# Optimization experiments

Hardware: AMD Instinct MI355X
Metric: run time of the kernel (lower is better)

The kernel has to match this reference:

```python
import jax, jax.numpy as jnp
import numpy as np

B, S, D, H = 4, 2048, 2048, 16
HD = D // H  # 128
THETA = 10000.0


def setup_inputs() -> dict:
    key = jax.random.key(0)
    k1, k2, k3 = jax.random.split(key, 3)
    x = jax.random.normal(k1, (B, S, D), dtype=jnp.float32)
    wqkv = jax.random.normal(k2, (3 * D, D), dtype=jnp.float32) * (1.0 / np.sqrt(D))
    wo = jax.random.normal(k3, (D, D), dtype=jnp.float32) * (1.0 / np.sqrt(D))
    return {"x": x, "wqkv": wqkv, "wo": wo}


def _rotate_half(t):
    t1 = t[..., : t.shape[-1] // 2]
    t2 = t[..., t.shape[-1] // 2 :]
    return jnp.concatenate([-t2, t1], axis=-1)


def reference(x, wqkv, wo):
    b, s, d = x.shape
    h, hd = H, HD
    # fused QKV projection (Linear without bias: x @ W^T)
    qkv = jnp.einsum("bsd,ed->bse", x, wqkv).reshape(b, s, 3, h, hd)
    xq, xk, xv = qkv[:, :, 0], qkv[:, :, 1], qkv[:, :, 2]

    # RoPE tables (start_pos = 0)
    inv_freq = 1.0 / (THETA ** (jnp.arange(0, hd, 2, dtype=jnp.float32) / hd))
    t = jnp.arange(s, dtype=jnp.float32)
    freqs = jnp.outer(t, inv_freq)  # [s, hd/2]
    cos = jnp.concatenate([jnp.cos(freqs)] * 2, axis=-1).reshape(1, s, 1, hd)
    sin = jnp.concatenate([jnp.sin(freqs)] * 2, axis=-1).reshape(1, s, 1, hd)

    xq = xq * cos + _rotate_half(xq) * sin
    xk = xk * cos + _rotate_half(xk) * sin

    # causal SDPA (kv_cache is None, seq_len > 1)
    scale = 1.0 / np.sqrt(hd)
    scores = jnp.einsum("bqhd,bkhd->bhqk", xq, xk) * scale
    causal = jnp.tril(jnp.ones((s, s), dtype=bool))
    scores = jnp.where(causal, scores, jnp.finfo(scores.dtype).min)
    attn = jax.nn.softmax(scores, axis=-1)
    out = jnp.einsum("bhqk,bkhd->bqhd", attn, xv).reshape(b, s, d)
    return jnp.einsum("bsd,od->bso", out, wo)
```

## Files before the change

kernel.cpp:

```cpp
#include <hip/hip_runtime.h>

typedef unsigned short u16;
typedef unsigned int u32;
typedef __bf16 bf16x8 __attribute__((ext_vector_type(8)));
typedef unsigned short u16x8 __attribute__((ext_vector_type(8)));
typedef float f32x4 __attribute__((ext_vector_type(4)));

#define S_LEN 2048
#define NH 16
#define HD 128

#define AS1 __attribute__((address_space(1)))
#define AS3 __attribute__((address_space(3)))

__device__ __forceinline__ u16 f2bf(float x) {
  u32 u = __builtin_bit_cast(u32, x);
  u32 r = u + 0x7FFFu + ((u >> 16) & 1u);
  return (u16)(r >> 16);
}
__device__ __forceinline__ float bf2f(u16 b) {
  return __builtin_bit_cast(float, (u32)b << 16);
}

__global__ void cvt_f32_bf16(const float* __restrict__ in, u16* __restrict__ out, int n4) {
  int i = blockIdx.x * 256 + threadIdx.x;
  if (i >= n4) return;
  float4 v = ((const float4*)in)[i];
  ushort4 o;
  o.x = f2bf(v.x); o.y = f2bf(v.y); o.z = f2bf(v.z); o.w = f2bf(v.w);
  ((ushort4*)out)[i] = o;
}

__global__ void build_tab(float* __restrict__ tab) {
  int t = blockIdx.x * 256 + threadIdx.x;
  int s = t >> 6, j = t & 63;
  float inv = exp2f(-(float)j * 0.20762050593045083f);
  float ang = (float)s * inv;
  tab[t] = cosf(ang);
  tab[131072 + t] = sinf(ang);
}

__device__ __forceinline__ void storeC(u16* p, float v) { *p = f2bf(v); }
__device__ __forceinline__ void storeC(float* p, float v) { *p = v; }

template <int EPI, typename OutT>
__global__ __launch_bounds__(512, 2) void gemm_fused(const u16* __restrict__ A, const u16* __restrict__ B,
                                                     OutT* __restrict__ C, const float* __restrict__ tab,
                                                     u16* __restrict__ Qr, u16* __restrict__ Kr,
                                                     u16* __restrict__ Vt,
                                                     int M, int N, int K, int nbx) {
  __shared__ alignas(16) u16 LDS[65536];
  char* lds = (char*)LDS;
  const int tid = threadIdx.x;
  const int lane = tid & 63;
  const int w = tid >> 6;
  const int wr = w >> 2, wc = w & 3;
  const int g = lane >> 4, c = lane & 15;

  const int nwg = gridDim.x;
  const int id = blockIdx.x;
  const int sw = (id & 7) * (nwg >> 3) + (id >> 3);
  const int bx = sw % nbx, by = sw / nbx;
  const size_t rowBase = (size_t)by * 256;
  const size_t colBase = (size_t)bx * 256;

  const int half = w & 1;
  const int sub = (w >> 1) & 3;
  const size_t ldb = (size_t)K * 2;
  const int srow = lane >> 3;
  const int soff = ((lane & 7) ^ srow) << 4;
  const char* ApS = (const char*)A + (rowBase + half * 128 + srow) * ldb + soff;
  const char* BpS = (const char*)B + (colBase + half * 128 + srow) * ldb + soff;

  auto stA = [&](int u, int blk) {
    const int r0 = blk * 32 + sub * 8;
    const int dst = ((u & 1) * 2 + half) * 16384 + r0 * 128;
    __builtin_amdgcn_global_load_lds((const AS1 void*)(ApS + (size_t)r0 * ldb + (size_t)u * 128),
                                     (AS3 void*)(lds + dst), 16, 0, 0);
  };
  auto stB = [&](int u, int jj) {
    const int r0 = (sub * 4 + jj) * 8;
    const int dst = 65536 + ((u & 1) * 2 + half) * 16384 + r0 * 128;
    __builtin_amdgcn_global_load_lds((const AS1 void*)(BpS + (size_t)r0 * ldb + (size_t)u * 128),
                                     (AS3 void*)(lds + dst), 16, 0, 0);
  };

  const int dq32 = (wc & 1) * 32;
  const int swz = (c & 7) << 4;
  auto rdA = [&](int bA, int mi, int kk) -> bf16x8 {
    return *(const bf16x8*)(lds + bA + mi * 2048 + c * 128 + ((kk * 64 + g * 16) ^ swz));
  };
  auto rdB = [&](int bB, int n, int kk) -> bf16x8 {
    int row_l;
    if (EPI) row_l = dq32 + (n & 1) * 16 + ((n >= 2) ? 64 : 0) + c;
    else     row_l = (wc & 1) * 64 + n * 16 + c;
    return *(const bf16x8*)(lds + bB + row_l * 128 + ((kk * 64 + g * 16) ^ swz));
  };

  f32x4 acc[8][4];
#pragma unroll
  for (int m = 0; m < 8; ++m)
#pragma unroll
    for (int n = 0; n < 4; ++n) acc[m][n] = f32x4{0.f, 0.f, 0.f, 0.f};

  bf16x8 bf_[4][2];
  bf16x8 aP[4], aQ[4];

  auto loadA = [&](bf16x8 (&s)[4], int bA, int mi) {
    s[0] = rdA(bA, mi, 0); s[1] = rdA(bA, mi, 1);
    s[2] = rdA(bA, mi + 1, 0); s[3] = rdA(bA, mi + 1, 1);
  };
  auto loadR1 = [&](int bA, int bB) {
    loadA(aP, bA, 0);
#pragma unroll
    for (int n = 0; n < 4; ++n) { bf_[n][0] = rdB(bB, n, 0); bf_[n][1] = rdB(bB, n, 1); }
  };
  auto MFMA2 = [&](int mi, bf16x8 (&s)[4]) {
#pragma unroll
    for (int n = 0; n < 4; ++n) {
      acc[mi][n]     = __builtin_amdgcn_mfma_f32_16x16x32_bf16(s[0], bf_[n][0], acc[mi][n], 0, 0, 0);
      acc[mi][n]     = __builtin_amdgcn_mfma_f32_16x16x32_bf16(s[1], bf_[n][1], acc[mi][n], 0, 0, 0);
      acc[mi + 1][n] = __builtin_amdgcn_mfma_f32_16x16x32_bf16(s[2], bf_[n][0], acc[mi + 1][n], 0, 0, 0);
      acc[mi + 1][n] = __builtin_amdgcn_mfma_f32_16x16x32_bf16(s[3], bf_[n][1], acc[mi + 1][n], 0, 0, 0);
    }
  };

  const int NT = K >> 6;

#pragma unroll
  for (int b = 0; b < 4; ++b) stA(0, b);
#pragma unroll
  for (int j = 0; j < 4; ++j) stB(0, j);
#pragma unroll
  for (int b = 0; b < 4; ++b) stA(1, b);
#pragma unroll
  for (int j = 0; j < 4; ++j) stB(1, j);
  asm volatile("s_waitcnt vmcnt(8)" ::: "memory");
  __builtin_amdgcn_s_barrier();
  {
    const int bA0 = wr * 16384;
    const int bB0 = 65536 + (wc >> 1) * 16384;
    loadR1(bA0, bB0);
  }

#pragma unroll 1
  for (int t = 0; t < NT; ++t) {
    const int bA = (t & 1) * 32768 + wr * 16384;
    const int bB = 65536 + (t & 1) * 32768 + (wc >> 1) * 16384;
    loadA(aQ, bA, 2);
    if (t >= 1 && t + 1 < NT) stA(t + 1, 3);
    asm volatile("s_waitcnt lgkmcnt(4)" ::: "memory");
    __builtin_amdgcn_sched_barrier(0);
    __builtin_amdgcn_s_setprio(1);
    MFMA2(0, aP);
    __builtin_amdgcn_s_setprio(0);
    __builtin_amdgcn_sched_barrier(0);
    __builtin_amdgcn_s_barrier();
    loadA(aP, bA, 4);
    if (t + 2 < NT) { stA(t + 2, 0); stB(t + 2, 0); stB(t + 2, 1); }
    asm volatile("s_waitcnt lgkmcnt(4)" ::: "memory");
    __builtin_amdgcn_sched_barrier(0);
    __builtin_amdgcn_s_setprio(1);
    MFMA2(2, aQ);
    __builtin_amdgcn_s_setprio(0);
    __builtin_amdgcn_sched_barrier(0);
    __builtin_amdgcn_s_barrier();
    loadA(aQ, bA, 6);
    if (t + 2 < NT) { stA(t + 2, 1); stB(t + 2, 2); stB(t + 2, 3); }
    asm volatile("s_waitcnt lgkmcnt(4)" ::: "memory");
    __builtin_amdgcn_sched_barrier(0);
    __builtin_amdgcn_s_setprio(1);
    MFMA2(4, aP);
    __builtin_amdgcn_s_setprio(0);
    __builtin_amdgcn_sched_barrier(0);
    __builtin_amdgcn_s_barrier();
    if (t + 2 < NT) stA(t + 2, 2);
    asm volatile("s_waitcnt lgkmcnt(0)" ::: "memory");
    __builtin_amdgcn_sched_barrier(0);
    __builtin_amdgcn_s_setprio(1);
    MFMA2(6, aQ);
    __builtin_amdgcn_s_setprio(0);
    __builtin_amdgcn_sched_barrier(0);
    if (t + 2 < NT) { asm volatile("s_waitcnt vmcnt(7)" ::: "memory"); }
    else            { asm volatile("s_waitcnt vmcnt(0)" ::: "memory"); }
    __builtin_amdgcn_s_barrier();
    if (t + 1 < NT) {
      const int bA1 = ((t + 1) & 1) * 32768 + wr * 16384;
      const int bB1 = 65536 + ((t + 1) & 1) * 32768 + (wc >> 1) * 16384;
      loadR1(bA1, bB1);
    }
  }

  if (EPI == 0) {
#pragma unroll
    for (int m = 0; m < 8; ++m)
#pragma unroll
      for (int n = 0; n < 4; ++n) {
        size_t row = rowBase + wr * 128 + m * 16 + g * 4;
        size_t col = colBase + wc * 64 + n * 16 + c;
#pragma unroll
        for (int r = 0; r < 4; ++r)
          storeC(&C[(row + r) * (size_t)N + col], acc[m][n][r]);
      }
  } else {
    const int slot = (int)(colBase >> 11);
    const int h = (((int)colBase >> 7) & 15) + (wc >> 1);
    const int bidx = (int)(rowBase >> 11);
    const int sbase = ((int)rowBase & 2047) + wr * 128;

    if (slot < 2) {
      u16* dst = (slot == 0 ? Qr : Kr) + (size_t)(bidx * NH + h) * S_LEN * HD;
#pragma unroll
      for (int m = 0; m < 8; ++m)
#pragma unroll
        for (int r = 0; r < 4; ++r) {
          const int s = sbase + m * 16 + g * 4 + r;
          u16* drow = dst + (size_t)s * HD;
          const float* tc = tab + s * 64;
          const float* ts = tab + 131072 + s * 64;
#pragma unroll
          for (int n = 0; n < 2; ++n) {
            const int dlo = dq32 + n * 16 + c;
            float cs = tc[dlo], sn = ts[dlo];
            float xlo = acc[m][n][r], xhi = acc[m][n + 2][r];
            drow[dlo]      = f2bf(cs * xlo - sn * xhi);
            drow[dlo + 64] = f2bf(cs * xhi + sn * xlo);
          }
        }
    } else {
      char* lv = lds + w * 16384;
#pragma unroll
      for (int m = 0; m < 8; ++m)
#pragma unroll
        for (int n = 0; n < 4; ++n) {
          const int ld = ((n >= 2) ? 32 : 0) + (n & 1) * 16 + c;
          ushort4 pk;
          pk.x = f2bf(acc[m][n][0]); pk.y = f2bf(acc[m][n][1]);
          pk.z = f2bf(acc[m][n][2]); pk.w = f2bf(acc[m][n][3]);
          *(ushort4*)(lv + ld * 256 + ((m * 32 + g * 8) ^ ((ld & 7) << 4))) = pk;
        }
      u16* vbase = Vt + (size_t)(bidx * NH + h) * HD * S_LEN;
#pragma unroll
      for (int rr = 0; rr < 16; ++rr) {
        const int ld = rr * 4 + (lane >> 4);
        const int d = dq32 + ld + ((rr >= 8) ? 32 : 0);
        u16x8 v = *(const u16x8*)(lv + ld * 256 + (((lane & 15) * 16) ^ ((ld & 7) << 4)));
        *(u16x8*)(vbase + (size_t)d * S_LEN + sbase + (lane & 15) * 8) = v;
      }
    }
  }
}

__global__ __launch_bounds__(512, 4) void attn_fwd(const u16* __restrict__ Q, const u16* __restrict__ K,
                                                   const u16* __restrict__ Vt, u16* __restrict__ O) {
  __shared__ alignas(16) u16 Ks[2 * 64 * 128];
  __shared__ alignas(16) u16 Vs[2 * 128 * 64];
  __shared__ alignas(16) u16 Pl[8 * 16 * 64];
  const int tid = threadIdx.x;
  const int lane = tid & 63;
  const int w = tid >> 6;
  const int g = lane >> 4, c = lane & 15;
  const int bh = blockIdx.x;
  const int pair = blockIdx.y;
  const int b = bh >> 4, h = bh & 15;

  const u16* Qb = Q + (size_t)bh * S_LEN * HD;
  const u16* Kb = K + (size_t)bh * S_LEN * HD;
  const u16* Vb = Vt + (size_t)bh * HD * S_LEN;
  const float SL = 0.12751753f;
  const int swz = (c & 7) << 4;

  int ldsOff[2], srcK[2], srcV[2];
#pragma unroll
  for (int ii = 0; ii < 2; ++ii) {
    int p = (w * 2 + ii) * 1024 + lane * 16;
    ldsOff[ii] = p;
    int rk = p >> 8, ik = p & 255;
    srcK[ii] = rk * 256 + (ik ^ ((rk & 7) << 4));
    int rv = p >> 7, iv = p & 127;
    srcV[ii] = rv * (S_LEN * 2) + (iv ^ ((rv & 7) << 4));
  }
  int koff[4], voff[2];
#pragma unroll
  for (int kb = 0; kb < 4; ++kb) koff[kb] = (kb * 64 + g * 16) ^ swz;
  voff[0] = (g * 16) ^ swz;
  voff[1] = (64 + g * 16) ^ swz;
  int poff[4];
#pragma unroll
  for (int t = 0; t < 4; ++t) poff[t] = (t * 32 + g * 8) ^ swz;
  char* Pw = (char*)Pl + w * 2048;

#pragma unroll 1
  for (int ph = 0; ph < 2; ++ph) {
    const int sti = ph ? (15 - pair) : pair;
    const int qb0 = sti * 128;
    const int q0 = qb0 + w * 16;

    bf16x8 qf[4];
#pragma unroll
    for (int kb = 0; kb < 4; ++kb)
      qf[kb] = *(const bf16x8*)&Qb[(size_t)(q0 + c) * HD + kb * 32 + g * 8];

    f32x4 acc[8];
#pragma unroll
    for (int cb = 0; cb < 8; ++cb) acc[cb] = f32x4{0.f, 0.f, 0.f, 0.f};
    float m_i = -3e38f, l_i = 0.f;

    const int nsteps = sti * 2 + 2;
#pragma unroll
    for (int ii = 0; ii < 2; ++ii) {
      __builtin_amdgcn_global_load_lds((const AS1 void*)((const char*)Kb + srcK[ii]),
                                       (AS3 void*)((char*)Ks + ldsOff[ii] - lane * 16), 16, 0, 0);
      __builtin_amdgcn_global_load_lds((const AS1 void*)((const char*)Vb + srcV[ii]),
                                       (AS3 void*)((char*)Vs + ldsOff[ii] - lane * 16), 16, 0, 0);
    }
    __syncthreads();
    int cur = 0;

#pragma unroll 1
    for (int st = 0; st < nsteps; ++st) {
      const int kv0 = st << 6;
      if (st + 1 < nsteps) {
        const char* kbase = (const char*)Kb + (size_t)(kv0 + 64) * 256;
        const char* vbase = (const char*)Vb + (size_t)(kv0 + 64) * 2;
        const int nb = (cur ^ 1) * 16384;
#pragma unroll
        for (int ii = 0; ii < 2; ++ii) {
          __builtin_amdgcn_global_load_lds((const AS1 void*)(kbase + srcK[ii]),
                                           (AS3 void*)((char*)Ks + nb + ldsOff[ii] - lane * 16), 16, 0, 0);
          __builtin_amdgcn_global_load_lds((const AS1 void*)(vbase + srcV[ii]),
                                           (AS3 void*)((char*)Vs + nb + ldsOff[ii] - lane * 16), 16, 0, 0);
        }
      }
      if (kv0 < q0 + 16) {
        const char* Kt = (const char*)Ks + cur * 16384;
        const char* Vtl = (const char*)Vs + cur * 16384;
        f32x4 s[4];
#pragma unroll
        for (int t = 0; t < 4; ++t) s[t] = f32x4{0.f, 0.f, 0.f, 0.f};
#pragma unroll
        for (int t = 0; t < 4; ++t)
#pragma unroll
          for (int kb = 0; kb < 4; ++kb) {
            bf16x8 kf = *(const bf16x8*)(Kt + t * 4096 + c * 256 + koff[kb]);
            s[t] = __builtin_amdgcn_mfma_f32_16x16x32_bf16(kf, qf[kb], s[t], 0, 0, 0);
          }
        if (kv0 + 63 > q0) {
          const int lim = q0 + c - kv0 - 4 * g;
#pragma unroll
          for (int t = 0; t < 4; ++t)
#pragma unroll
            for (int r = 0; r < 4; ++r)
              s[t][r] = (16 * t + r <= lim) ? s[t][r] : -3e38f;
        }
        float mx = s[0][0];
#pragma unroll
        for (int t = 0; t < 4; ++t)
#pragma unroll
          for (int r = 0; r < 4; ++r) mx = fmaxf(mx, s[t][r]);
        mx = fmaxf(mx, __shfl_xor(mx, 16));
        mx = fmaxf(mx, __shfl_xor(mx, 32));
        const float mn = fmaxf(m_i, mx);
        const float alpha = exp2f((m_i - mn) * SL);
        float rs = 0.f;
#pragma unroll
        for (int t = 0; t < 4; ++t) {
          float p0 = exp2f((s[t][0] - mn) * SL);
          float p1 = exp2f((s[t][1] - mn) * SL);
          float p2 = exp2f((s[t][2] - mn) * SL);
          float p3 = exp2f((s[t][3] - mn) * SL);
          rs += (p0 + p1) + (p2 + p3);
          ushort4 pw;
          pw.x = f2bf(p0); pw.y = f2bf(p1); pw.z = f2bf(p2); pw.w = f2bf(p3);
          *(ushort4*)(Pw + c * 128 + poff[t]) = pw;
        }
        rs += __shfl_xor(rs, 16);
        rs += __shfl_xor(rs, 32);
        l_i = l_i * alpha + rs;
        m_i = mn;
        float ar[4];
#pragma unroll
        for (int r = 0; r < 4; ++r) ar[r] = __shfl(alpha, 4 * g + r);
#pragma unroll
        for (int cb = 0; cb < 8; ++cb)
#pragma unroll
          for (int r = 0; r < 4; ++r) acc[cb][r] *= ar[r];
        bf16x8 pa0 = *(const bf16x8*)(Pw + c * 128 + voff[0]);
        bf16x8 pa1 = *(const bf16x8*)(Pw + c * 128 + voff[1]);
#pragma unroll
        for (int cb = 0; cb < 8; ++cb) {
          bf16x8 vf0 = *(const bf16x8*)(Vtl + cb * 2048 + c * 128 + voff[0]);
          acc[cb] = __builtin_amdgcn_mfma_f32_16x16x32_bf16(pa0, vf0, acc[cb], 0, 0, 0);
          bf16x8 vf1 = *(const bf16x8*)(Vtl + cb * 2048 + c * 128 + voff[1]);
          acc[cb] = __builtin_amdgcn_mfma_f32_16x16x32_bf16(pa1, vf1, acc[cb], 0, 0, 0);
        }
      }
      __syncthreads();
      cur ^= 1;
    }
    float linv = 1.0f / l_i;
    float lr[4];
#pragma unroll
    for (int r = 0; r < 4; ++r) lr[r] = __shfl(linv, 4 * g + r);
#pragma unroll
    for (int cb = 0; cb < 8; ++cb)
#pragma unroll
      for (int r = 0; r < 4; ++r) {
        int q = q0 + 4 * g + r;
        O[(((size_t)b * S_LEN + q) * NH + h) * HD + cb * 16 + c] = f2bf(acc[cb][r] * lr[r]);
      }
  }
}

extern "C" void kernel_launch(void* const* d_in, const int* in_sizes, int n_in,
                              void* d_out, int out_size, void* d_ws, size_t ws_size,
                              hipStream_t stream) {
  const float* x    = (const float*)d_in[0];
  const float* wqkv = (const float*)d_in[1];
  const float* wo   = (const float*)d_in[2];
  float* out = (float*)d_out;
  char* ws = (char*)d_ws;

  u16*  xb    = (u16*)(ws + 0);
  u16*  wqkvb = (u16*)(ws + 33554432);
  float* tab  = (float*)(ws + 58720256);
  u16*  wob   = (u16*)(ws + 58720256);
  u16*  Vt    = (u16*)(ws + 167772160);
  u16*  attn  = (u16*)(ws + 0);
  u16*  Qr = (u16*)d_out;
  u16*  Kr = (u16*)d_out + 16777216;

  cvt_f32_bf16<<<16384, 256, 0, stream>>>(x, xb, 16777216 / 4);
  cvt_f32_bf16<<<12288, 256, 0, stream>>>(wqkv, wqkvb, 12582912 / 4);
  build_tab<<<512, 256, 0, stream>>>(tab);

  gemm_fused<1, u16><<<768, 512, 0, stream>>>(xb, wqkvb, (u16*)nullptr, tab, Qr, Kr, Vt,
                                              8192, 6144, 2048, 24);

  cvt_f32_bf16<<<4096, 256, 0, stream>>>(wo, wob, 4194304 / 4);

  attn_fwd<<<dim3(64, 8), 512, 0, stream>>>(Qr, Kr, Vt, attn);

  gemm_fused<0, float><<<256, 512, 0, stream>>>(attn, wob, out, nullptr, nullptr, nullptr, nullptr,
                                                8192, 2048, 2048, 8);
}
```

Measured before the change: 406.0 us.

## Process 32 query rows per wave in attention and merge input conversions

Each attention wave now handles two 16-row query tiles (256 queries per block), so every K/V fragment read from LDS feeds twice as many MFMAs. The grid is halved to 64x4 and launch bounds drop to 2 blocks per CU to allow the doubled accumulator and register state. Separately, the x and wqkv fp32-to-bf16 conversions are merged into one launch. The change trades occupancy and parallelism (only 256 blocks, coarser causal balancing) for better K/V reuse and fewer launches.

Measured after the change: 404.5 us (median of 4 runs). Within noise of the previous version (-0.4%).

```diff
diff --git a/kernel.cpp b/kernel.cpp
--- a/kernel.cpp
+++ b/kernel.cpp
@@ -20,6 +20,18 @@
 }
 __device__ __forceinline__ float bf2f(u16 b) {
   return __builtin_bit_cast(float, (u32)b << 16);
+}
+
+__global__ void cvt_xw(const float* __restrict__ x, const float* __restrict__ wq,
+                       u16* __restrict__ xb, u16* __restrict__ wqb) {
+  int i = blockIdx.x * 256 + threadIdx.x;
+  const float* src; u16* dst;
+  if (i < 4194304) { src = x; dst = xb; }
+  else { i -= 4194304; src = wq; dst = wqb; }
+  float4 v = ((const float4*)src)[i];
+  ushort4 o;
+  o.x = f2bf(v.x); o.y = f2bf(v.y); o.z = f2bf(v.z); o.w = f2bf(v.w);
+  ((ushort4*)dst)[i] = o;
 }
 
 __global__ void cvt_f32_bf16(const float* __restrict__ in, u16* __restrict__ out, int n4) {
@@ -251,11 +263,11 @@
   }
 }
 
-__global__ __launch_bounds__(512, 4) void attn_fwd(const u16* __restrict__ Q, const u16* __restrict__ K,
+__global__ __launch_bounds__(512, 2) void attn_fwd(const u16* __restrict__ Q, const u16* __restrict__ K,
                                                    const u16* __restrict__ Vt, u16* __restrict__ O) {
   __shared__ alignas(16) u16 Ks[2 * 64 * 128];
   __shared__ alignas(16) u16 Vs[2 * 128 * 64];
-  __shared__ alignas(16) u16 Pl[8 * 16 * 64];
+  __shared__ alignas(16) u16 Pl[8 * 32 * 64];
   const int tid = threadIdx.x;
   const int lane = tid & 63;
   const int w = tid >> 6;
@@ -288,25 +300,28 @@
   int poff[4];
 #pragma unroll
   for (int t = 0; t < 4; ++t) poff[t] = (t * 32 + g * 8) ^ swz;
-  char* Pw = (char*)Pl + w * 2048;
+  char* Pw = (char*)Pl + w * 4096;
 
 #pragma unroll 1
   for (int ph = 0; ph < 2; ++ph) {
-    const int sti = ph ? (15 - pair) : pair;
-    const int qb0 = sti * 128;
-    const int q0 = qb0 + w * 16;
-
-    bf16x8 qf[4];
-#pragma unroll
-    for (int kb = 0; kb < 4; ++kb)
-      qf[kb] = *(const bf16x8*)&Qb[(size_t)(q0 + c) * HD + kb * 32 + g * 8];
-
-    f32x4 acc[8];
-#pragma unroll
-    for (int cb = 0; cb < 8; ++cb) acc[cb] = f32x4{0.f, 0.f, 0.f, 0.f};
-    float m_i = -3e38f, l_i = 0.f;
-
-    const int nsteps = sti * 2 + 2;
+    const int sti = ph ? (7 - pair) : pair;
+    const int q0 = sti * 256 + w * 32;
+
+    bf16x8 qf[2][4];
+#pragma unroll
+    for (int qh = 0; qh < 2; ++qh)
+#pragma unroll
+      for (int kb = 0; kb < 4; ++kb)
+        qf[qh][kb] = *(const bf16x8*)&Qb[(size_t)(q0 + qh * 16 + c) * HD + kb * 32 + g * 8];
+
+    f32x4 acc[2][8];
+#pragma unroll
+    for (int qh = 0; qh < 2; ++qh)
+#pragma unroll
+      for (int cb = 0; cb < 8; ++cb) acc[qh][cb] = f32x4{0.f, 0.f, 0.f, 0.f};
+    float m_i[2] = {-3e38f, -3e38f}, l_i[2] = {0.f, 0.f};
+
+    const int nsteps = sti * 4 + 4;
 #pragma unroll
     for (int ii = 0; ii < 2; ++ii) {
       __builtin_amdgcn_global_load_lds((const AS1 void*)((const char*)Kb + srcK[ii]),
@@ -332,83 +347,103 @@
                                            (AS3 void*)((char*)Vs + nb + ldsOff[ii] - lane * 16), 16, 0, 0);
         }
       }
-      if (kv0 < q0 + 16) {
+      if (kv0 < q0 + 32) {
         const char* Kt = (const char*)Ks + cur * 16384;
         const char* Vtl = (const char*)Vs + cur * 16384;
-        f32x4 s[4];
-#pragma unroll
-        for (int t = 0; t < 4; ++t) s[t] = f32x4{0.f, 0.f, 0.f, 0.f};
+        f32x4 s[2][4];
+#pragma unroll
+        for (int qh = 0; qh < 2; ++qh)
+#pragma unroll
+          for (int t = 0; t < 4; ++t) s[qh][t] = f32x4{0.f, 0.f, 0.f, 0.f};
 #pragma unroll
         for (int t = 0; t < 4; ++t)
 #pragma unroll
           for (int kb = 0; kb < 4; ++kb) {
             bf16x8 kf = *(const bf16x8*)(Kt + t * 4096 + c * 256 + koff[kb]);
-            s[t] = __builtin_amdgcn_mfma_f32_16x16x32_bf16(kf, qf[kb], s[t], 0, 0, 0);
+            s[0][t] = __builtin_amdgcn_mfma_f32_16x16x32_bf16(kf, qf[0][kb], s[0][t], 0, 0, 0);
+            s[1][t] = __builtin_amdgcn_mfma_f32_16x16x32_bf16(kf, qf[1][kb], s[1][t], 0, 0, 0);
           }
         if (kv0 + 63 > q0) {
-          const int lim = q0 + c - kv0 - 4 * g;
+#pragma unroll
+          for (int qh = 0; qh < 2; ++qh) {
+            const int lim = q0 + qh * 16 + c - kv0 - 4 * g;
+#pragma unroll
+            for (int t = 0; t < 4; ++t)
+#pragma unroll
+              for (int r = 0; r < 4; ++r)
+                s[qh][t][r] = (16 * t + r <= lim) ? s[qh][t][r] : -3e38f;
+          }
+        }
+        float ar[2][4];
+#pragma unroll
+        for (int qh = 0; qh < 2; ++qh) {
+          float mx = s[qh][0][0];
 #pragma unroll
           for (int t = 0; t < 4; ++t)
 #pragma unroll
-            for (int r = 0; r < 4; ++r)
-              s[t][r] = (16 * t + r <= lim) ? s[t][r] : -3e38f;
-        }
-        float mx = s[0][0];
-#pragma unroll
-        for (int t = 0; t < 4; ++t)
-#pragma unroll
-          for (int r = 0; r < 4; ++r) mx = fmaxf(mx, s[t][r]);
-        mx = fmaxf(mx, __shfl_xor(mx, 16));
-        mx = fmaxf(mx, __shfl_xor(mx, 32));
-        const float mn = fmaxf(m_i, mx);
-        const float alpha = exp2f((m_i - mn) * SL);
-        float rs = 0.f;
-#pragma unroll
-        for (int t = 0; t < 4; ++t) {
-          float p0 = exp2f((s[t][0] - mn) * SL);
-          float p1 = exp2f((s[t][1] - mn) * SL);
-          float p2 = exp2f((s[t][2] - mn) * SL);
-          float p3 = exp2f((s[t][3] - mn) * SL);
-          rs += (p0 + p1) + (p2 + p3);
-          ushort4 pw;
-          pw.x = f2bf(p0); pw.y = f2bf(p1); pw.z = f2bf(p2); pw.w = f2bf(p3);
-          *(ushort4*)(Pw + c * 128 + poff[t]) = pw;
-        }
-        rs += __shfl_xor(rs, 16);
-        rs += __shfl_xor(rs, 32);
-        l_i = l_i * alpha + rs;
-        m_i = mn;
-        float ar[4];
-#pragma unroll
-        for (int r = 0; r < 4; ++r) ar[r] = __shfl(alpha, 4 * g + r);
-#pragma unroll
-        for (int cb = 0; cb < 8; ++cb)
-#pragma unroll
-          for (int r = 0; r < 4; ++r) acc[cb][r] *= ar[r];
-        bf16x8 pa0 = *(const bf16x8*)(Pw + c * 128 + voff[0]);
-        bf16x8 pa1 = *(const bf16x8*)(Pw + c * 128 + voff[1]);
+            for (int r = 0; r < 4; ++r) mx = fmaxf(mx, s[qh][t][r]);
+          mx = fmaxf(mx, __shfl_xor(mx, 16));
+          mx = fmaxf(mx, __shfl_xor(mx, 32));
+          const float mn = fmaxf(m_i[qh], mx);
+          const float alpha = exp2f((m_i[qh] - mn) * SL);
+          float rs = 0.f;
+#pragma unroll
+          for (int t = 0; t < 4; ++t) {
+            float p0 = exp2f((s[qh][t][0] - mn) * SL);
+            float p1 = exp2f((s[qh][t][1] - mn) * SL);
+            float p2 = exp2f((s[qh][t][2] - mn) * SL);
+            float p3 = exp2f((s[qh][t][3] - mn) * SL);
+            rs += (p0 + p1) + (p2 + p3);
+            ushort4 pw;
+            pw.x = f2bf(p0); pw.y = f2bf(p1); pw.z = f2bf(p2); pw.w = f2bf(p3);
+            *(ushort4*)(Pw + (qh * 16 + c) * 128 + poff[t]) = pw;
+          }
+          rs += __shfl_xor(rs, 16);
+          rs += __shfl_xor(rs, 32);
+          l_i[qh] = l_i[qh] * alpha + rs;
+          m_i[qh] = mn;
+#pragma unroll
+          for (int r = 0; r < 4; ++r) ar[qh][r] = __shfl(alpha, 4 * g + r);
+        }
+#pragma unroll
+        for (int qh = 0; qh < 2; ++qh)
+#pragma unroll
+          for (int cb = 0; cb < 8; ++cb)
+#pragma unroll
+            for (int r = 0; r < 4; ++r) acc[qh][cb][r] *= ar[qh][r];
+        bf16x8 pa[2][2];
+#pragma unroll
+        for (int qh = 0; qh < 2; ++qh) {
+          pa[qh][0] = *(const bf16x8*)(Pw + (qh * 16 + c) * 128 + voff[0]);
+          pa[qh][1] = *(const bf16x8*)(Pw + (qh * 16 + c) * 128 + voff[1]);
+        }
 #pragma unroll
         for (int cb = 0; cb < 8; ++cb) {
           bf16x8 vf0 = *(const bf16x8*)(Vtl + cb * 2048 + c * 128 + voff[0]);
-          acc[cb] = __builtin_amdgcn_mfma_f32_16x16x32_bf16(pa0, vf0, acc[cb], 0, 0, 0);
           bf16x8 vf1 = *(const bf16x8*)(Vtl + cb * 2048 + c * 128 + voff[1]);
-          acc[cb] = __builtin_amdgcn_mfma_f32_16x16x32_bf16(pa1, vf1, acc[cb], 0, 0, 0);
+          acc[0][cb] = __builtin_amdgcn_mfma_f32_16x16x32_bf16(pa[0][0], vf0, acc[0][cb], 0, 0, 0);
+          acc[0][cb] = __builtin_amdgcn_mfma_f32_16x16x32_bf16(pa[0][1], vf1, acc[0][cb], 0, 0, 0);
+          acc[1][cb] = __builtin_amdgcn_mfma_f32_16x16x32_bf16(pa[1][0], vf0, acc[1][cb], 0, 0, 0);
+          acc[1][cb] = __builtin_amdgcn_mfma_f32_16x16x32_bf16(pa[1][1], vf1, acc[1][cb], 0, 0, 0);
         }
       }
       __syncthreads();
       cur ^= 1;
     }
-    float linv = 1.0f / l_i;
-    float lr[4];
-#pragma unroll
-    for (int r = 0; r < 4; ++r) lr[r] = __shfl(linv, 4 * g + r);
-#pragma unroll
-    for (int cb = 0; cb < 8; ++cb)
-#pragma unroll
-      for (int r = 0; r < 4; ++r) {
-        int q = q0 + 4 * g + r;
-        O[(((size_t)b * S_LEN + q) * NH + h) * HD + cb * 16 + c] = f2bf(acc[cb][r] * lr[r]);
-      }
+#pragma unroll
+    for (int qh = 0; qh < 2; ++qh) {
+      float linv = 1.0f / l_i[qh];
+      float lr[4];
+#pragma unroll
+      for (int r = 0; r < 4; ++r) lr[r] = __shfl(linv, 4 * g + r);
+#pragma unroll
+      for (int cb = 0; cb < 8; ++cb)
+#pragma unroll
+        for (int r = 0; r < 4; ++r) {
+          int q = q0 + qh * 16 + 4 * g + r;
+          O[(((size_t)b * S_LEN + q) * NH + h) * HD + cb * 16 + c] = f2bf(acc[qh][cb][r] * lr[r]);
+        }
+    }
   }
 }
 
@@ -430,8 +465,7 @@
   u16*  Qr = (u16*)d_out;
   u16*  Kr = (u16*)d_out + 16777216;
 
-  cvt_f32_bf16<<<16384, 256, 0, stream>>>(x, xb, 16777216 / 4);
-  cvt_f32_bf16<<<12288, 256, 0, stream>>>(wqkv, wqkvb, 12582912 / 4);
+  cvt_xw<<<28672, 256, 0, stream>>>(x, wqkv, xb, wqkvb);
   build_tab<<<512, 256, 0, stream>>>(tab);
 
   gemm_fused<1, u16><<<768, 512, 0, stream>>>(xb, wqkvb, (u16*)nullptr, tab, Qr, Kr, Vt,
@@ -439,7 +473,7 @@
 
   cvt_f32_bf16<<<4096, 256, 0, stream>>>(wo, wob, 4194304 / 4);
 
-  attn_fwd<<<dim3(64, 8), 512, 0, stream>>>(Qr, Kr, Vt, attn);
+  attn_fwd<<<dim3(64, 4), 512, 0, stream>>>(Qr, Kr, Vt, attn);
 
   gemm_fused<0, float><<<256, 512, 0, stream>>>(attn, wob, out, nullptr, nullptr, nullptr, nullptr,
                                                 8192, 2048, 2048, 8);
```
